# Performance work log

Hardware: AMD Instinct MI355X
Metric: run time of the kernel (lower is better)

## Reference

```python
import math
import jax, jax.numpy as jnp
import numpy as np

T, N, D = 8, 1024, 128  # num_timestamps, tot_nodes, node_input_size

def setup_inputs() -> dict:
    key = jax.random.key(0)
    k1, k2 = jax.random.split(key)
    raw_features = jax.random.normal(k1, (T, N, D), dtype=jnp.float32)
    adj = jax.random.randint(k2, (N, N), 0, 2, dtype=jnp.int32)
    return {"raw_features": raw_features, "adj": adj}

def reference(raw_features, adj):
    t, n, d = raw_features.shape
    scale = 1.0 / math.sqrt(d)
    # --- GAT: adjacency-masked self-attention per timestamp ---
    scores = jnp.einsum('tnd,tmd->tnm', raw_features, raw_features) * scale  # [T,N,N]
    masked = jnp.where(adj[None] > 0, scores, jnp.float32(-1e12))
    attention = jax.nn.softmax(masked, axis=2)
    node_features = jnp.einsum('tnm,tmd->tnd', attention, raw_features)      # [T,N,D]
    # --- temporal scores per node ---
    spatial_features = node_features.transpose(1, 0, 2)                      # [N,T,D]
    temp_scores = jnp.einsum('ntd,nsd->nts', spatial_features, spatial_features) * scale
    spatial_weights = jax.nn.sigmoid(temp_scores)                            # [N,T,T]
    # --- repeat(N,1,1).view(N,N,T,T) == broadcast over leading axis: ST[i,j] = sw[j] ---
    ST = jnp.broadcast_to(spatial_weights[None], (n, n, t, t))               # [N,N,T,T]
    ST = ST.transpose(3, 1, 2, 0)                                            # [T,N,T,N]
    return ST.reshape(t * n, t * n)
```

## Files before the change

### kernel.cpp

```cpp
#include <hip/hip_runtime.h>
#include <hip/hip_bf16.h>
#include <math.h>

#define T 8
#define N 1024
#define D 128

constexpr float SCALE = 0.08838834764831845f;

typedef __attribute__((ext_vector_type(8))) short short8;
typedef __attribute__((ext_vector_type(4))) float floatx4;

#define MFMA16(a, b, c) __builtin_amdgcn_mfma_f32_16x16x32_bf16((a), (b), (c), 0, 0, 0)

__global__ __launch_bounds__(256) void convert_bf16(const float* __restrict__ X,
                                                    ushort* __restrict__ XB,
                                                    ushort* __restrict__ XBT_hi,
                                                    ushort* __restrict__ XBT_lo) {
    const int t  = blockIdx.y;
    const int n0 = blockIdx.x * 64;
    const int tid = threadIdx.x;

    __shared__ ushort Hi[128][66];
    __shared__ ushort Lo[128][66];

    #pragma unroll
    for (int r = 0; r < 8; ++r) {
        int idx = r * 256 + tid;
        int nl  = idx >> 5;
        int c4  = idx & 31;
        float4 v = *(const float4*)(X + ((size_t)t * N + n0 + nl) * D + c4 * 4);
        float vv[4] = {v.x, v.y, v.z, v.w};
        ushort4 o; ushort* op = (ushort*)&o;
        #pragma unroll
        for (int k = 0; k < 4; ++k) {
            __hip_bfloat16 h = __float2bfloat16(vv[k]);
            float hf = __bfloat162float(h);
            __hip_bfloat16 l = __float2bfloat16(vv[k] - hf);
            op[k] = *(ushort*)&h;
            Hi[c4 * 4 + k][nl] = *(ushort*)&h;
            Lo[c4 * 4 + k][nl] = *(ushort*)&l;
        }
        *(ushort4*)(XB + ((size_t)t * N + n0 + nl) * D + c4 * 4) = o;
    }
    __syncthreads();

    const int u  = tid & 31;
    const int dr = tid >> 5;
    #pragma unroll
    for (int p = 0; p < 16; ++p) {
        int d = p * 8 + dr;
        uint hv = *(const uint*)&Hi[d][2 * u];
        uint lv = *(const uint*)&Lo[d][2 * u];
        size_t off = ((size_t)t * D + d) * N + n0 + 2 * u;
        *(uint*)(XBT_hi + off) = hv;
        *(uint*)(XBT_lo + off) = lv;
    }
}

__global__ __launch_bounds__(256) void pack_adj(const int* __restrict__ adj,
                                                ushort* __restrict__ Abits) {
    int g = blockIdx.x * 256 + threadIdx.x;
    int i = g >> 6, w = g & 63;
    const int4* p4 = (const int4*)(adj + (size_t)i * N + w * 16);
    uint m16 = 0;
    #pragma unroll
    for (int v4 = 0; v4 < 4; ++v4) {
        int4 v = p4[v4];
        m16 |= (v.x != 0 ? 1u : 0u) << (v4 * 4 + 0);
        m16 |= (v.y != 0 ? 1u : 0u) << (v4 * 4 + 1);
        m16 |= (v.z != 0 ? 1u : 0u) << (v4 * 4 + 2);
        m16 |= (v.w != 0 ? 1u : 0u) << (v4 * 4 + 3);
    }
    Abits[g] = (ushort)m16;
}

__global__ __launch_bounds__(256, 2) void attn_fused(const ushort* __restrict__ XB,
                                                     const ushort* __restrict__ XBT_hi,
                                                     const ushort* __restrict__ XBT_lo,
                                                     const ushort* __restrict__ Abits,
                                                     float* __restrict__ NF) {
    const int g  = blockIdx.x;
    const int t  = g & 7;
    const int i0 = (g >> 3) * 16;
    const int tid  = threadIdx.x;
    const int wid  = tid >> 6;
    const int lane = tid & 63;
    const int m    = lane & 15;
    const int quad = lane >> 4;
    const int jbase = wid * 256;

    __shared__ ushort Ph[16][1024];
    __shared__ ushort Plo[16][1024];
    float* red = (float*)&Ph[0][0];

    const ushort* Xt = XB + (size_t)t * N * D;

    short8 afrag[4];
    {
        const ushort* pa = Xt + (size_t)(i0 + m) * D + quad * 8;
        #pragma unroll
        for (int kq = 0; kq < 4; ++kq) afrag[kq] = *(const short8*)(pa + kq * 32);
    }

    floatx4 acc[16];
    #pragma unroll
    for (int c = 0; c < 16; ++c) acc[c] = (floatx4){0.f, 0.f, 0.f, 0.f};

    short8 bfr[2][4];
    {
        const ushort* pb = Xt + (size_t)(jbase + m) * D + quad * 8;
        bfr[0][0] = *(const short8*)(pb);
        bfr[0][1] = *(const short8*)(pb + 32);
        bfr[0][2] = *(const short8*)(pb + 64);
        bfr[0][3] = *(const short8*)(pb + 96);
    }
    #pragma unroll
    for (int c = 0; c < 16; ++c) {
        if (c < 15) {
            const ushort* pb = Xt + (size_t)(jbase + 16 * (c + 1) + m) * D + quad * 8;
            bfr[(c + 1) & 1][0] = *(const short8*)(pb);
            bfr[(c + 1) & 1][1] = *(const short8*)(pb + 32);
            bfr[(c + 1) & 1][2] = *(const short8*)(pb + 64);
            bfr[(c + 1) & 1][3] = *(const short8*)(pb + 96);
        }
        acc[c] = MFMA16(afrag[0], bfr[c & 1][0], acc[c]);
        acc[c] = MFMA16(afrag[1], bfr[c & 1][1], acc[c]);
        acc[c] = MFMA16(afrag[2], bfr[c & 1][2], acc[c]);
        acc[c] = MFMA16(afrag[3], bfr[c & 1][3], acc[c]);
    }

    short8 adjw[4][2];
    #pragma unroll
    for (int q = 0; q < 4; ++q) {
        const ushort* ap = Abits + (size_t)(i0 + quad * 4 + q) * 64 + wid * 16;
        adjw[q][0] = *(const short8*)ap;
        adjw[q][1] = *(const short8*)(ap + 8);
    }
    #pragma unroll
    for (int q = 0; q < 4; ++q) {
        #pragma unroll
        for (int c = 0; c < 16; ++c) {
            int aw = (ushort)((c < 8) ? adjw[q][0][c] : adjw[q][1][c - 8]);
            acc[c][q] = ((aw >> m) & 1) ? acc[c][q] * SCALE : -1e12f;
        }
    }

    float mx[4], inv[4];
    #pragma unroll
    for (int q = 0; q < 4; ++q) {
        float v_ = acc[0][q];
        #pragma unroll
        for (int c = 1; c < 16; ++c) v_ = fmaxf(v_, acc[c][q]);
        v_ = fmaxf(v_, __shfl_xor(v_, 1));
        v_ = fmaxf(v_, __shfl_xor(v_, 2));
        v_ = fmaxf(v_, __shfl_xor(v_, 4));
        v_ = fmaxf(v_, __shfl_xor(v_, 8));
        mx[q] = v_;
    }
    if (m == 0) {
        #pragma unroll
        for (int q = 0; q < 4; ++q) red[wid * 16 + quad * 4 + q] = mx[q];
    }
    __syncthreads();
    #pragma unroll
    for (int q = 0; q < 4; ++q) {
        int r = quad * 4 + q;
        mx[q] = fmaxf(fmaxf(red[r], red[16 + r]), fmaxf(red[32 + r], red[48 + r]));
    }

    float sm[4];
    #pragma unroll
    for (int q = 0; q < 4; ++q) {
        float s_ = 0.f;
        #pragma unroll
        for (int c = 0; c < 16; ++c) {
            float p = __expf(acc[c][q] - mx[q]);
            acc[c][q] = p;
            s_ += p;
        }
        s_ += __shfl_xor(s_, 1);
        s_ += __shfl_xor(s_, 2);
        s_ += __shfl_xor(s_, 4);
        s_ += __shfl_xor(s_, 8);
        sm[q] = s_;
    }
    if (m == 0) {
        #pragma unroll
        for (int q = 0; q < 4; ++q) red[64 + wid * 16 + quad * 4 + q] = sm[q];
    }
    __syncthreads();
    #pragma unroll
    for (int q = 0; q < 4; ++q) {
        int r = quad * 4 + q;
        inv[q] = 1.f / (red[64 + r] + red[80 + r] + red[96 + r] + red[112 + r]);
    }
    __syncthreads();

    #pragma unroll
    for (int q = 0; q < 4; ++q) {
        const int row = quad * 4 + q;
        #pragma unroll
        for (int c = 0; c < 16; ++c) {
            const int col = jbase + 16 * c + m;
            const int sc = ((((col >> 3) ^ (row & 7)) << 3) | (col & 7));
            float p = acc[c][q] * inv[q];
            __hip_bfloat16 h = __float2bfloat16(p);
            float hf = __bfloat162float(h);
            __hip_bfloat16 l = __float2bfloat16(p - hf);
            Ph[row][sc]  = *(ushort*)&h;
            Plo[row][sc] = *(ushort*)&l;
        }
    }
    __syncthreads();

    const ushort* rowh[2];
    const ushort* rowl[2];
    const int f0 = wid * 32;
    #pragma unroll
    for (int nt = 0; nt < 2; ++nt) {
        size_t rb = ((size_t)t * D + f0 + nt * 16 + m) * N;
        rowh[nt] = XBT_hi + rb;
        rowl[nt] = XBT_lo + rb;
    }
    short8 pfh[4][2], pfl[4][2];
#define PF(kq_)                                                                  \
    {                                                                            \
        const int off_ = (kq_) * 32 + quad * 8;                                  \
        pfh[(kq_) & 3][0] = *(const short8*)(rowh[0] + off_);                    \
        pfh[(kq_) & 3][1] = *(const short8*)(rowh[1] + off_);                    \
        pfl[(kq_) & 3][0] = *(const short8*)(rowl[0] + off_);                    \
        pfl[(kq_) & 3][1] = *(const short8*)(rowl[1] + off_);                    \
    }
    PF(0); PF(1); PF(2);

    floatx4 accN[2];
    accN[0] = (floatx4){0.f, 0.f, 0.f, 0.f};
    accN[1] = (floatx4){0.f, 0.f, 0.f, 0.f};
    #pragma unroll
    for (int kq = 0; kq < 32; ++kq) {
        if (kq < 29) PF(kq + 3);
        const int blk = (((kq * 4 + quad) ^ (m & 7)) << 3);
        short8 ah = *(const short8*)&Ph[m][blk];
        short8 al = *(const short8*)&Plo[m][blk];
        #pragma unroll
        for (int nt = 0; nt < 2; ++nt) {
            accN[nt] = MFMA16(ah, pfh[kq & 3][nt], accN[nt]);
            accN[nt] = MFMA16(ah, pfl[kq & 3][nt], accN[nt]);
            accN[nt] = MFMA16(al, pfh[kq & 3][nt], accN[nt]);
        }
    }
#undef PF

    float* NFt = NF + (size_t)t * N * D;
    #pragma unroll
    for (int nt = 0; nt < 2; ++nt)
        #pragma unroll
        for (int q = 0; q < 4; ++q)
            NFt[(size_t)(i0 + quad * 4 + q) * D + f0 + nt * 16 + m] = accN[nt][q];
}

__global__ __launch_bounds__(256) void expand_fused(const float* __restrict__ NF,
                                                    float* __restrict__ out) {
    const int row = blockIdx.x;
    const int b = row >> 10, j = row & 1023;
    const int tid = threadIdx.x;

    __shared__ float F[T][D + 4];
    __shared__ float w[T];

    {
        int a = tid >> 5, c4 = (tid & 31) * 4;
        *(float4*)(&F[a][c4]) = *(const float4*)(NF + ((size_t)a * N + j) * D + c4);
    }
    __syncthreads();

    if (tid < T) {
        float s = 0.f;
        #pragma unroll
        for (int d4 = 0; d4 < 32; ++d4) {
            float4 fa = *(const float4*)(&F[tid][d4 * 4]);
            float4 fb = *(const float4*)(&F[b][d4 * 4]);
            s += fa.x * fb.x + fa.y * fb.y + fa.z * fb.z + fa.w * fb.w;
        }
        w[tid] = 1.f / (1.f + __expf(-s * SCALE));
    }
    __syncthreads();

    floatx4* orow = (floatx4*)(out + (size_t)row * (T * N));
    #pragma unroll
    for (int a = 0; a < T; ++a) {
        float wv = w[a];
        floatx4 v = {wv, wv, wv, wv};
        __builtin_nontemporal_store(v, orow + a * 256 + tid);
    }
}

extern "C" void kernel_launch(void* const* d_in, const int* in_sizes, int n_in,
                              void* d_out, int out_size, void* d_ws, size_t ws_size,
                              hipStream_t stream) {
    const float* X   = (const float*)d_in[0];
    const int*   adj = (const int*)d_in[1];
    float* out = (float*)d_out;

    float*  NF     = (float*)d_ws;
    ushort* XB     = (ushort*)(NF + (size_t)T * N * D);
    ushort* XBT_hi = XB + (size_t)T * N * D;
    ushort* XBT_lo = XBT_hi + (size_t)T * N * D;
    ushort* Abits  = XBT_lo + (size_t)T * N * D;

    convert_bf16<<<dim3(N / 64, T), 256, 0, stream>>>(X, XB, XBT_hi, XBT_lo);
    pack_adj<<<dim3(N * 64 / 256), 256, 0, stream>>>(adj, Abits);
    attn_fused<<<dim3((N / 16) * T), 256, 0, stream>>>(XB, XBT_hi, XBT_lo, Abits, NF);
    expand_fused<<<dim3(T * N), 256, 0, stream>>>(NF, out);
}
```

Baseline: 325.6 us.

## Double attention waves per block and block the transposed feature layout for coalescing

attn_fused now runs 8 waves per block instead of 4. Each wave scores 128 key columns and produces one 16-wide output feature tile, which roughly halves per-thread accumulators and raises occupancy. The transposed hi/lo bf16 copies of X are stored in a blocked [t][n/8][d][8] layout, so the PV-stage B-fragment loads become contiguous 16-byte chunks across lanes instead of row-strided reads. The cost is more cross-wave reduction traffic for the softmax max/sum and more block-level synchronization per block.

New measurement: 308.1 us (median of 2 runs). 1.06x faster.

```diff
diff --git a/kernel.cpp b/kernel.cpp
--- a/kernel.cpp
+++ b/kernel.cpp
@@ -52,7 +52,10 @@
         int d = p * 8 + dr;
         uint hv = *(const uint*)&Hi[d][2 * u];
         uint lv = *(const uint*)&Lo[d][2 * u];
-        size_t off = ((size_t)t * D + d) * N + n0 + 2 * u;
+        int n_lo = 2 * u;
+        int g8   = (n0 + n_lo) >> 3;
+        int pos  = n_lo & 7;
+        size_t off = (((size_t)t * 128 + g8) * 128 + d) * 8 + pos;
         *(uint*)(XBT_hi + off) = hv;
         *(uint*)(XBT_lo + off) = lv;
     }
@@ -75,7 +78,7 @@
     Abits[g] = (ushort)m16;
 }
 
-__global__ __launch_bounds__(256, 2) void attn_fused(const ushort* __restrict__ XB,
+__global__ __launch_bounds__(512, 4) void attn_fused(const ushort* __restrict__ XB,
                                                      const ushort* __restrict__ XBT_hi,
                                                      const ushort* __restrict__ XBT_lo,
                                                      const ushort* __restrict__ Abits,
@@ -88,7 +91,7 @@
     const int lane = tid & 63;
     const int m    = lane & 15;
     const int quad = lane >> 4;
-    const int jbase = wid * 256;
+    const int jbase = wid * 128;
 
     __shared__ ushort Ph[16][1024];
     __shared__ ushort Plo[16][1024];
@@ -103,9 +106,9 @@
         for (int kq = 0; kq < 4; ++kq) afrag[kq] = *(const short8*)(pa + kq * 32);
     }
 
-    floatx4 acc[16];
-    #pragma unroll
-    for (int c = 0; c < 16; ++c) acc[c] = (floatx4){0.f, 0.f, 0.f, 0.f};
+    floatx4 acc[8];
+    #pragma unroll
+    for (int c = 0; c < 8; ++c) acc[c] = (floatx4){0.f, 0.f, 0.f, 0.f};
 
     short8 bfr[2][4];
     {
@@ -116,8 +119,8 @@
         bfr[0][3] = *(const short8*)(pb + 96);
     }
     #pragma unroll
-    for (int c = 0; c < 16; ++c) {
-        if (c < 15) {
+    for (int c = 0; c < 8; ++c) {
+        if (c < 7) {
             const ushort* pb = Xt + (size_t)(jbase + 16 * (c + 1) + m) * D + quad * 8;
             bfr[(c + 1) & 1][0] = *(const short8*)(pb);
             bfr[(c + 1) & 1][1] = *(const short8*)(pb + 32);
@@ -130,18 +133,15 @@
         acc[c] = MFMA16(afrag[3], bfr[c & 1][3], acc[c]);
     }
 
-    short8 adjw[4][2];
-    #pragma unroll
-    for (int q = 0; q < 4; ++q) {
-        const ushort* ap = Abits + (size_t)(i0 + quad * 4 + q) * 64 + wid * 16;
-        adjw[q][0] = *(const short8*)ap;
-        adjw[q][1] = *(const short8*)(ap + 8);
-    }
-    #pragma unroll
-    for (int q = 0; q < 4; ++q) {
-        #pragma unroll
-        for (int c = 0; c < 16; ++c) {
-            int aw = (ushort)((c < 8) ? adjw[q][0][c] : adjw[q][1][c - 8]);
+    short8 adjw[4];
+    #pragma unroll
+    for (int q = 0; q < 4; ++q)
+        adjw[q] = *(const short8*)(Abits + (size_t)(i0 + quad * 4 + q) * 64 + wid * 8);
+    #pragma unroll
+    for (int q = 0; q < 4; ++q) {
+        #pragma unroll
+        for (int c = 0; c < 8; ++c) {
+            int aw = (ushort)adjw[q][c];
             acc[c][q] = ((aw >> m) & 1) ? acc[c][q] * SCALE : -1e12f;
         }
     }
@@ -151,7 +151,7 @@
     for (int q = 0; q < 4; ++q) {
         float v_ = acc[0][q];
         #pragma unroll
-        for (int c = 1; c < 16; ++c) v_ = fmaxf(v_, acc[c][q]);
+        for (int c = 1; c < 8; ++c) v_ = fmaxf(v_, acc[c][q]);
         v_ = fmaxf(v_, __shfl_xor(v_, 1));
         v_ = fmaxf(v_, __shfl_xor(v_, 2));
         v_ = fmaxf(v_, __shfl_xor(v_, 4));
@@ -166,7 +166,10 @@
     #pragma unroll
     for (int q = 0; q < 4; ++q) {
         int r = quad * 4 + q;
-        mx[q] = fmaxf(fmaxf(red[r], red[16 + r]), fmaxf(red[32 + r], red[48 + r]));
+        float v_ = red[r];
+        #pragma unroll
+        for (int w = 1; w < 8; ++w) v_ = fmaxf(v_, red[w * 16 + r]);
+        mx[q] = v_;
     }
 
     float sm[4];
@@ -174,7 +177,7 @@
     for (int q = 0; q < 4; ++q) {
         float s_ = 0.f;
         #pragma unroll
-        for (int c = 0; c < 16; ++c) {
+        for (int c = 0; c < 8; ++c) {
             float p = __expf(acc[c][q] - mx[q]);
             acc[c][q] = p;
             s_ += p;
@@ -187,13 +190,16 @@
     }
     if (m == 0) {
         #pragma unroll
-        for (int q = 0; q < 4; ++q) red[64 + wid * 16 + quad * 4 + q] = sm[q];
+        for (int q = 0; q < 4; ++q) red[128 + wid * 16 + quad * 4 + q] = sm[q];
     }
     __syncthreads();
     #pragma unroll
     for (int q = 0; q < 4; ++q) {
         int r = quad * 4 + q;
-        inv[q] = 1.f / (red[64 + r] + red[80 + r] + red[96 + r] + red[112 + r]);
+        float s_ = red[128 + r];
+        #pragma unroll
+        for (int w = 1; w < 8; ++w) s_ += red[128 + w * 16 + r];
+        inv[q] = 1.f / s_;
     }
     __syncthreads();
 
@@ -201,7 +207,7 @@
     for (int q = 0; q < 4; ++q) {
         const int row = quad * 4 + q;
         #pragma unroll
-        for (int c = 0; c < 16; ++c) {
+        for (int c = 0; c < 8; ++c) {
             const int col = jbase + 16 * c + m;
             const int sc = ((((col >> 3) ^ (row & 7)) << 3) | (col & 7));
             float p = acc[c][q] * inv[q];
@@ -214,50 +220,35 @@
     }
     __syncthreads();
 
-    const ushort* rowh[2];
-    const ushort* rowl[2];
-    const int f0 = wid * 32;
-    #pragma unroll
-    for (int nt = 0; nt < 2; ++nt) {
-        size_t rb = ((size_t)t * D + f0 + nt * 16 + m) * N;
-        rowh[nt] = XBT_hi + rb;
-        rowl[nt] = XBT_lo + rb;
-    }
-    short8 pfh[4][2], pfl[4][2];
+    const int dcol = wid * 16 + m;
+    const ushort* ph_base = XBT_hi + (size_t)t * 131072 + (size_t)dcol * 8;
+    const ushort* pl_base = XBT_lo + (size_t)t * 131072 + (size_t)dcol * 8;
+    short8 pfh[4], pfl[4];
 #define PF(kq_)                                                                  \
     {                                                                            \
-        const int off_ = (kq_) * 32 + quad * 8;                                  \
-        pfh[(kq_) & 3][0] = *(const short8*)(rowh[0] + off_);                    \
-        pfh[(kq_) & 3][1] = *(const short8*)(rowh[1] + off_);                    \
-        pfl[(kq_) & 3][0] = *(const short8*)(rowl[0] + off_);                    \
-        pfl[(kq_) & 3][1] = *(const short8*)(rowl[1] + off_);                    \
+        const size_t off_ = (size_t)((kq_) * 4 + quad) * 1024;                   \
+        pfh[(kq_) & 3] = *(const short8*)(ph_base + off_);                       \
+        pfl[(kq_) & 3] = *(const short8*)(pl_base + off_);                       \
     }
     PF(0); PF(1); PF(2);
 
-    floatx4 accN[2];
-    accN[0] = (floatx4){0.f, 0.f, 0.f, 0.f};
-    accN[1] = (floatx4){0.f, 0.f, 0.f, 0.f};
+    floatx4 accN = (floatx4){0.f, 0.f, 0.f, 0.f};
     #pragma unroll
     for (int kq = 0; kq < 32; ++kq) {
         if (kq < 29) PF(kq + 3);
         const int blk = (((kq * 4 + quad) ^ (m & 7)) << 3);
         short8 ah = *(const short8*)&Ph[m][blk];
         short8 al = *(const short8*)&Plo[m][blk];
-        #pragma unroll
-        for (int nt = 0; nt < 2; ++nt) {
-            accN[nt] = MFMA16(ah, pfh[kq & 3][nt], accN[nt]);
-            accN[nt] = MFMA16(ah, pfl[kq & 3][nt], accN[nt]);
-            accN[nt] = MFMA16(al, pfh[kq & 3][nt], accN[nt]);
-        }
+        accN = MFMA16(ah, pfh[kq & 3], accN);
+        accN = MFMA16(ah, pfl[kq & 3], accN);
+        accN = MFMA16(al, pfh[kq & 3], accN);
     }
 #undef PF
 
     float* NFt = NF + (size_t)t * N * D;
     #pragma unroll
-    for (int nt = 0; nt < 2; ++nt)
-        #pragma unroll
-        for (int q = 0; q < 4; ++q)
-            NFt[(size_t)(i0 + quad * 4 + q) * D + f0 + nt * 16 + m] = accN[nt][q];
+    for (int q = 0; q < 4; ++q)
+        NFt[(size_t)(i0 + quad * 4 + q) * D + dcol] = accN[q];
 }
 
 __global__ __launch_bounds__(256) void expand_fused(const float* __restrict__ NF,
@@ -311,6 +302,6 @@
 
     convert_bf16<<<dim3(N / 64, T), 256, 0, stream>>>(X, XB, XBT_hi, XBT_lo);
     pack_adj<<<dim3(N * 64 / 256), 256, 0, stream>>>(adj, Abits);
-    attn_fused<<<dim3((N / 16) * T), 256, 0, stream>>>(XB, XBT_hi, XBT_lo, Abits, NF);
+    attn_fused<<<dim3((N / 16) * T), 512, 0, stream>>>(XB, XBT_hi, XBT_lo, Abits, NF);
     expand_fused<<<dim3(T * N), 256, 0, stream>>>(NF, out);
 }
```
